# Kernel tuning notes

Measured on AMD Instinct MI355X. Metric: run time of the kernel, lower is better.

The kernel has to match this reference:

```python
import jax, jax.numpy as jnp
import numpy as np

B, D = 4096, 1024
NA, NNEG = 2048, 4094
L2_WEIGHT = 0.005


def setup_inputs() -> dict:
    key = jax.random.key(0)
    k1, k2, k3, k4 = jax.random.split(key, 4)
    batch = jax.random.normal(k1, (B, D), dtype=jnp.float32)
    anchors = jax.random.randint(k2, (NA,), 0, B)
    positives = jax.random.randint(k3, (NA,), 0, B)
    negatives = jax.random.randint(k4, (NA, NNEG), 0, B)
    return {"batch": batch, "anchors": anchors, "positives": positives, "negatives": negatives}


def reference(batch, anchors, positives, negatives):
    # a . (n - p) = a.n - a.p  -> one GEMM against the whole batch, then gathers.
    a_embs = batch[anchors]                       # [Na, D]
    scores = a_embs @ batch.T                     # [Na, B]
    pos = jnp.take_along_axis(scores, positives[:, None], axis=1)   # [Na, 1]
    neg = jnp.take_along_axis(scores, negatives, axis=1)            # [Na, Nneg]
    inner = neg - pos                             # [Na, Nneg]
    npair = jnp.mean(jnp.log(jnp.sum(jnp.exp(inner), axis=1) + 1.0))
    # per-anchor l2 term: l2_weight * mean(||batch||) added len(anchors) times / len(anchors)
    l2 = L2_WEIGHT * jnp.mean(jnp.linalg.norm(batch, axis=1))
    return npair + l2
```

## Files before the change

kernel.cpp:

```cpp
#include <hip/hip_runtime.h>
#include <hip/hip_bf16.h>
#include <math.h>

constexpr int kB    = 4096;
constexpr int kD    = 1024;
constexpr int kNA   = 2048;
constexpr int kNNEG = 4094;
constexpr float kL2W = 0.005f;


typedef __attribute__((ext_vector_type(8))) int   int8v;
typedef __attribute__((ext_vector_type(4))) int   int4v;
typedef __attribute__((ext_vector_type(4))) float f32x4;

__device__ inline void async_load16(const void* g, void* l) {
    __builtin_amdgcn_global_load_lds(
        (const __attribute__((address_space(1))) unsigned*)g,
        (__attribute__((address_space(3))) unsigned*)l, 16, 0, 0);
}
__device__ inline float bf16_to_f(unsigned short u) {
    union { unsigned int i; float f; } c; c.i = ((unsigned int)u) << 16; return c.f;
}

__global__ __launch_bounds__(256) void conv_norms_kernel(
    const float* __restrict__ batch,
    unsigned char* __restrict__ f8,
    float* __restrict__ norms)
{
    const int row = blockIdx.x, t = threadIdx.x;
    const float4 v = ((const float4*)(batch + (size_t)row * kD))[t];
    unsigned int p = __builtin_amdgcn_cvt_pk_fp8_f32(v.x, v.y, 0, false);
    p = __builtin_amdgcn_cvt_pk_fp8_f32(v.z, v.w, p, true);
    ((unsigned int*)(f8 + (size_t)row * kD))[t] = p;

    float acc = v.x * v.x + v.y * v.y + v.z * v.z + v.w * v.w;
    __shared__ float s[4];
    const int lane = t & 63, wid = t >> 6;
#pragma unroll
    for (int o2 = 32; o2; o2 >>= 1) acc += __shfl_down(acc, o2);
    if (lane == 0) s[wid] = acc;
    __syncthreads();
    if (t == 0) norms[row] = sqrtf(s[0] + s[1] + s[2] + s[3]);
}

__global__ __launch_bounds__(256) void gemm_mfma_kernel(
    const unsigned char* __restrict__ f8,
    const int*           __restrict__ anchors,
    unsigned short*      __restrict__ scores)
{
    __shared__ __align__(16) char As[128 * 128];
    __shared__ __align__(16) char Bs[128 * 128];
    __shared__ int aid[128];

    const int t  = threadIdx.x;
    const int w  = t >> 6;
    const int l  = t & 63;
    const int m0 = blockIdx.y * 128;
    const int n0 = blockIdx.x * 128;

    if (t < 128) aid[t] = anchors[m0 + t];
    __syncthreads();

    const unsigned char* gA[4];
    const unsigned char* gB[4];
    int slot[4];
#pragma unroll
    for (int i = 0; i < 4; ++i) {
        const int idx = i * 256 + t;
        const int row = idx >> 3;
        const int pc  = idx & 7;
        const int g   = pc ^ (row & 7);
        gA[i]   = f8 + (size_t)aid[row] * kD + g * 16;
        gB[i]   = f8 + (size_t)(n0 + row) * kD + g * 16;
        slot[i] = idx * 16;
    }

    const int wm = (w >> 1) * 64, wn = (w & 1) * 64;
    const int mr = l & 15, q = l >> 4;

    f32x4 acc[4][4] = {};

    for (int kt = 0; kt < kD; kt += 128) {
#pragma unroll
        for (int i = 0; i < 4; ++i) async_load16(gA[i] + kt, As + slot[i]);
#pragma unroll
        for (int i = 0; i < 4; ++i) async_load16(gB[i] + kt, Bs + slot[i]);
        __syncthreads();

        int8v a[4], b[4];
#pragma unroll
        for (int i = 0; i < 4; ++i) {
            int r  = wm + i * 16 + mr;
            int c0 = (2 * q) ^ (r & 7), c1 = (2 * q + 1) ^ (r & 7);
            int4v lo = *(const int4v*)(As + r * 128 + c0 * 16);
            int4v hi = *(const int4v*)(As + r * 128 + c1 * 16);
            a[i] = (int8v){lo.x, lo.y, lo.z, lo.w, hi.x, hi.y, hi.z, hi.w};
            r  = wn + i * 16 + mr;
            c0 = (2 * q) ^ (r & 7); c1 = (2 * q + 1) ^ (r & 7);
            lo = *(const int4v*)(Bs + r * 128 + c0 * 16);
            hi = *(const int4v*)(Bs + r * 128 + c1 * 16);
            b[i] = (int8v){lo.x, lo.y, lo.z, lo.w, hi.x, hi.y, hi.z, hi.w};
        }
#pragma unroll
        for (int i = 0; i < 4; ++i)
#pragma unroll
            for (int j = 0; j < 4; ++j)
                acc[i][j] = __builtin_amdgcn_mfma_scale_f32_16x16x128_f8f6f4(
                    a[i], b[j], acc[i][j],
                    0 , 0 ,
                    0, 0x7F ,
                    0, 0x7F );
        __syncthreads();
    }

#pragma unroll
    for (int i = 0; i < 4; ++i)
#pragma unroll
        for (int j = 0; j < 4; ++j)
#pragma unroll
            for (int r = 0; r < 4; ++r) {
                const int row = m0 + wm + i * 16 + q * 4 + r;
                const int col = n0 + wn + j * 16 + mr;
                __hip_bfloat16 h = __float2bfloat16(acc[i][j][r]);
                scores[(size_t)row * kB + col] = *(unsigned short*)&h;
            }
}

__global__ __launch_bounds__(256) void lse_kernel(
    const unsigned short* __restrict__ scores,
    const int*   __restrict__ positives,
    const int*   __restrict__ negatives,
    float*       __restrict__ lse)
{
    __shared__ unsigned short srow[kB];
    const int i = blockIdx.x;
    const int t = threadIdx.x;

    const uint4* grow = (const uint4*)(scores + (size_t)i * kB);
    ((uint4*)srow)[t]       = grow[t];
    ((uint4*)srow)[t + 256] = grow[t + 256];
    __syncthreads();

    const float pos = bf16_to_f(srow[positives[i]]);
    const int* negrow = negatives + (size_t)i * kNNEG;

    float v[16];
    float m = -INFINITY;
#pragma unroll
    for (int r = 0; r < 16; ++r) {
        const int j = t + 256 * r;
        v[r] = (j < kNNEG) ? (bf16_to_f(srow[negrow[j]]) - pos) : -INFINITY;
        m = fmaxf(m, v[r]);
    }

    __shared__ float sm[4], ss[4];
    const int lane = t & 63, wid = t >> 6;
#pragma unroll
    for (int o = 32; o; o >>= 1) m = fmaxf(m, __shfl_down(m, o));
    if (lane == 0) sm[wid] = m;
    __syncthreads();
    m = fmaxf(fmaxf(sm[0], sm[1]), fmaxf(sm[2], sm[3]));
    const float mp = fmaxf(m, 0.f);

    float acc = 0.f;
#pragma unroll
    for (int r = 0; r < 16; ++r) acc += expf(v[r] - mp);

#pragma unroll
    for (int o = 32; o; o >>= 1) acc += __shfl_down(acc, o);
    if (lane == 0) ss[wid] = acc;
    __syncthreads();
    if (t == 0)
        lse[i] = mp + logf(ss[0] + ss[1] + ss[2] + ss[3] + expf(-mp));
}

__global__ __launch_bounds__(256) void final_kernel(
    const float* __restrict__ lse,
    const float* __restrict__ norms,
    float*       __restrict__ out)
{
    float a = 0.f, b = 0.f;
    for (int i = threadIdx.x; i < kNA; i += 256) a += lse[i];
    for (int i = threadIdx.x; i < kB;  i += 256) b += norms[i];
    __shared__ float sa[4], sb[4];
    const int lane = threadIdx.x & 63, wid = threadIdx.x >> 6;
#pragma unroll
    for (int o = 32; o; o >>= 1) { a += __shfl_down(a, o); b += __shfl_down(b, o); }
    if (lane == 0) { sa[wid] = a; sb[wid] = b; }
    __syncthreads();
    if (threadIdx.x == 0) {
        const float npair = (sa[0] + sa[1] + sa[2] + sa[3]) / (float)kNA;
        const float l2    = kL2W * ((sb[0] + sb[1] + sb[2] + sb[3]) / (float)kB);
        out[0] = npair + l2;
    }
}

extern "C" void kernel_launch(void* const* d_in, const int* in_sizes, int n_in,
                              void* d_out, int out_size, void* d_ws, size_t ws_size,
                              hipStream_t stream)
{
    (void)in_sizes; (void)n_in; (void)out_size; (void)ws_size;

    const float* batch     = (const float*)d_in[0];
    const int*   anchors   = (const int*)d_in[1];
    const int*   positives = (const int*)d_in[2];
    const int*   negatives = (const int*)d_in[3];
    float*       out       = (float*)d_out;

    char* ws = (char*)d_ws;
    unsigned short* scores = (unsigned short*)ws;
    unsigned char*  f8     = (unsigned char*)(ws + (size_t)kNA * kB * 2);
    float*          lse    = (float*)(ws + (size_t)kNA * kB * 2 + (size_t)kB * kD);
    float*          norms  = lse + kNA;

    conv_norms_kernel<<<kB, 256, 0, stream>>>(batch, f8, norms);
    gemm_mfma_kernel<<<dim3(kB / 128, kNA / 128), 256, 0, stream>>>(f8, anchors, scores);
    lse_kernel<<<kNA, 256, 0, stream>>>(scores, positives, negatives, lse);
    final_kernel<<<1, 256, 0, stream>>>(lse, norms, out);
}
```

Baseline: 116.6 us.

## Fuse negative-weighted logsumexp into GEMM epilogue via per-anchor count histogram

Replaces the bf16 score matrix write and the gather-based LSE kernel with a per-anchor histogram of negative indices (uint8 counts), built in the same launch as the fp8 conversion. The GEMM epilogue then computes a count-weighted online max/sum-exp per row tile and emits partial (max, sum) pairs plus the positive score. A small merge kernel combines the partials and uses an atomic counter to do the final reduction. This removes the 16 MB score round-trip and the random gathers, at the cost of a heavier GEMM epilogue, shared-memory atomics and the assumption that each count fits in 8 bits.

```diff
diff --git a/kernel.cpp b/kernel.cpp
--- a/kernel.cpp
+++ b/kernel.cpp
@@ -18,35 +18,63 @@
         (const __attribute__((address_space(1))) unsigned*)g,
         (__attribute__((address_space(3))) unsigned*)l, 16, 0, 0);
 }
-__device__ inline float bf16_to_f(unsigned short u) {
-    union { unsigned int i; float f; } c; c.i = ((unsigned int)u) << 16; return c.f;
-}
-
-__global__ __launch_bounds__(256) void conv_norms_kernel(
+
+__global__ __launch_bounds__(256) void convhist_kernel(
     const float* __restrict__ batch,
+    const int*   __restrict__ negatives,
     unsigned char* __restrict__ f8,
-    float* __restrict__ norms)
-{
-    const int row = blockIdx.x, t = threadIdx.x;
-    const float4 v = ((const float4*)(batch + (size_t)row * kD))[t];
-    unsigned int p = __builtin_amdgcn_cvt_pk_fp8_f32(v.x, v.y, 0, false);
-    p = __builtin_amdgcn_cvt_pk_fp8_f32(v.z, v.w, p, true);
-    ((unsigned int*)(f8 + (size_t)row * kD))[t] = p;
-
-    float acc = v.x * v.x + v.y * v.y + v.z * v.z + v.w * v.w;
-    __shared__ float s[4];
-    const int lane = t & 63, wid = t >> 6;
-#pragma unroll
-    for (int o2 = 32; o2; o2 >>= 1) acc += __shfl_down(acc, o2);
-    if (lane == 0) s[wid] = acc;
-    __syncthreads();
-    if (t == 0) norms[row] = sqrtf(s[0] + s[1] + s[2] + s[3]);
+    unsigned char* __restrict__ cnt,
+    float* __restrict__ norms,
+    unsigned int* __restrict__ ctr)
+{
+    const int t = threadIdx.x;
+    if (blockIdx.x < kB) {
+        const int row = blockIdx.x;
+        const float4 v = ((const float4*)(batch + (size_t)row * kD))[t];
+        unsigned int p = __builtin_amdgcn_cvt_pk_fp8_f32(v.x, v.y, 0, false);
+        p = __builtin_amdgcn_cvt_pk_fp8_f32(v.z, v.w, p, true);
+        ((unsigned int*)(f8 + (size_t)row * kD))[t] = p;
+
+        float acc = v.x * v.x + v.y * v.y + v.z * v.z + v.w * v.w;
+        __shared__ float s[4];
+        const int lane = t & 63, wid = t >> 6;
+#pragma unroll
+        for (int o2 = 32; o2; o2 >>= 1) acc += __shfl_down(acc, o2);
+        if (lane == 0) s[wid] = acc;
+        __syncthreads();
+        if (t == 0) norms[row] = sqrtf(s[0] + s[1] + s[2] + s[3]);
+        if (blockIdx.x == 0 && t == 0) *ctr = 0;
+    } else {
+        const int i = blockIdx.x - kB;
+        __shared__ unsigned int h[kB];
+#pragma unroll
+        for (int r = 0; r < 16; ++r) h[t + 256 * r] = 0;
+        __syncthreads();
+        const int* negrow = negatives + (size_t)i * kNNEG;
+#pragma unroll
+        for (int r = 0; r < 16; ++r) {
+            const int j = t + 256 * r;
+            if (j < kNNEG) atomicAdd(&h[negrow[j]], 1u);
+        }
+        __syncthreads();
+        unsigned int w[4];
+#pragma unroll
+        for (int c = 0; c < 4; ++c) {
+            const int base = t * 16 + c * 4;
+            w[c] = (h[base] & 0xFFu) | ((h[base + 1] & 0xFFu) << 8) |
+                   ((h[base + 2] & 0xFFu) << 16) | ((h[base + 3] & 0xFFu) << 24);
+        }
+        ((uint4*)(cnt + (size_t)i * kB))[t] = make_uint4(w[0], w[1], w[2], w[3]);
+    }
 }
 
 __global__ __launch_bounds__(256) void gemm_mfma_kernel(
     const unsigned char* __restrict__ f8,
     const int*           __restrict__ anchors,
-    unsigned short*      __restrict__ scores)
+    const int*           __restrict__ positives,
+    const unsigned char* __restrict__ cnt,
+    float2*              __restrict__ part,
+    float*               __restrict__ posout)
 {
     __shared__ __align__(16) char As[128 * 128];
     __shared__ __align__(16) char Bs[128 * 128];
@@ -106,92 +134,111 @@
 #pragma unroll
             for (int j = 0; j < 4; ++j)
                 acc[i][j] = __builtin_amdgcn_mfma_scale_f32_16x16x128_f8f6f4(
-                    a[i], b[j], acc[i][j],
-                    0 , 0 ,
-                    0, 0x7F ,
-                    0, 0x7F );
-        __syncthreads();
-    }
-
-#pragma unroll
-    for (int i = 0; i < 4; ++i)
-#pragma unroll
-        for (int j = 0; j < 4; ++j)
-#pragma unroll
-            for (int r = 0; r < 4; ++r) {
-                const int row = m0 + wm + i * 16 + q * 4 + r;
-                const int col = n0 + wn + j * 16 + mr;
-                __hip_bfloat16 h = __float2bfloat16(acc[i][j][r]);
-                scores[(size_t)row * kB + col] = *(unsigned short*)&h;
+                    a[i], b[j], acc[i][j], 0, 0, 0, 0x7F, 0, 0x7F);
+        __syncthreads();
+    }
+
+    unsigned char* cntT = (unsigned char*)As;
+#pragma unroll
+    for (int i = 0; i < 4; ++i) {
+        const int idx = i * 256 + t;
+        const int row = idx >> 3;
+        const int c16 = idx & 7;
+        ((uint4*)cntT)[idx] =
+            *(const uint4*)(cnt + (size_t)(m0 + row) * kB + n0 + c16 * 16);
+    }
+    if (t < 128) aid[t] = positives[m0 + t];
+    __syncthreads();
+
+    float2* pm = (float2*)Bs;
+    const int half = wn >> 6;
+
+#pragma unroll
+    for (int i = 0; i < 4; ++i) {
+#pragma unroll
+        for (int r = 0; r < 4; ++r) {
+            const int rowL = wm + i * 16 + q * 4 + r;
+            float m4 = -1e30f;
+#pragma unroll
+            for (int j = 0; j < 4; ++j) {
+                const int colL = wn + j * 16 + mr;
+                const float s = acc[i][j][r];
+                if (cntT[rowL * 128 + colL] > 0) m4 = fmaxf(m4, s);
+                if (n0 + colL == aid[rowL]) posout[m0 + rowL] = s;
             }
-}
-
-__global__ __launch_bounds__(256) void lse_kernel(
-    const unsigned short* __restrict__ scores,
-    const int*   __restrict__ positives,
-    const int*   __restrict__ negatives,
-    float*       __restrict__ lse)
-{
-    __shared__ unsigned short srow[kB];
-    const int i = blockIdx.x;
+            float e4 = 0.f;
+#pragma unroll
+            for (int j = 0; j < 4; ++j) {
+                const int colL = wn + j * 16 + mr;
+                const float wgt = (float)cntT[rowL * 128 + colL];
+                const float e = (wgt > 0.f) ? __expf(acc[i][j][r] - m4) : 0.f;
+                e4 += wgt * e;
+            }
+            float M = m4, S = e4;
+#pragma unroll
+            for (int d = 1; d < 16; d <<= 1) {
+                const float Mo = __shfl_xor(M, d);
+                const float So = __shfl_xor(S, d);
+                const float Mn = fmaxf(M, Mo);
+                S = S * __expf(M - Mn) + So * __expf(Mo - Mn);
+                M = Mn;
+            }
+            if (mr == 0) pm[rowL * 2 + half] = make_float2(M, S);
+        }
+    }
+    __syncthreads();
+    if (t < 128) {
+        const float2 a0 = pm[t * 2], b0 = pm[t * 2 + 1];
+        const float M = fmaxf(a0.x, b0.x);
+        const float S = a0.y * __expf(a0.x - M) + b0.y * __expf(b0.x - M);
+        part[(size_t)(m0 + t) * 32 + blockIdx.x] = make_float2(M, S);
+    }
+}
+
+__global__ __launch_bounds__(256) void merge_kernel(
+    const float2* __restrict__ part,
+    const float*  __restrict__ posv,
+    const float*  __restrict__ norms,
+    float*        __restrict__ blocksums,
+    unsigned int* __restrict__ ctr,
+    float*        __restrict__ out)
+{
+    const int b = blockIdx.x;
     const int t = threadIdx.x;
 
-    const uint4* grow = (const uint4*)(scores + (size_t)i * kB);
-    ((uint4*)srow)[t]       = grow[t];
-    ((uint4*)srow)[t + 256] = grow[t + 256];
-    __syncthreads();
-
-    const float pos = bf16_to_f(srow[positives[i]]);
-    const int* negrow = negatives + (size_t)i * kNNEG;
-
-    float v[16];
-    float m = -INFINITY;
-#pragma unroll
-    for (int r = 0; r < 16; ++r) {
-        const int j = t + 256 * r;
-        v[r] = (j < kNNEG) ? (bf16_to_f(srow[negrow[j]]) - pos) : -INFINITY;
-        m = fmaxf(m, v[r]);
-    }
-
-    __shared__ float sm[4], ss[4];
+    float v = 0.f;
+    if (t < 128) {
+        const int row = b * 128 + t;
+        const float2* p = part + (size_t)row * 32;
+        float M = -1e30f;
+#pragma unroll
+        for (int c = 0; c < 32; ++c) M = fmaxf(M, p[c].x);
+        float S = 0.f;
+#pragma unroll
+        for (int c = 0; c < 32; ++c) S += p[c].y * __expf(p[c].x - M);
+        const float x = (M + logf(S)) - posv[row];
+        const float lse = (x > 0.f) ? (x + log1pf(__expf(-x))) : log1pf(__expf(x));
+        v = lse / (float)kNA;
+    }
+    v += kL2W * norms[b * 256 + t] / (float)kB;
+
+    __shared__ float s[4];
     const int lane = t & 63, wid = t >> 6;
 #pragma unroll
-    for (int o = 32; o; o >>= 1) m = fmaxf(m, __shfl_down(m, o));
-    if (lane == 0) sm[wid] = m;
-    __syncthreads();
-    m = fmaxf(fmaxf(sm[0], sm[1]), fmaxf(sm[2], sm[3]));
-    const float mp = fmaxf(m, 0.f);
-
-    float acc = 0.f;
-#pragma unroll
-    for (int r = 0; r < 16; ++r) acc += expf(v[r] - mp);
-
-#pragma unroll
-    for (int o = 32; o; o >>= 1) acc += __shfl_down(acc, o);
-    if (lane == 0) ss[wid] = acc;
-    __syncthreads();
-    if (t == 0)
-        lse[i] = mp + logf(ss[0] + ss[1] + ss[2] + ss[3] + expf(-mp));
-}
-
-__global__ __launch_bounds__(256) void final_kernel(
-    const float* __restrict__ lse,
-    const float* __restrict__ norms,
-    float*       __restrict__ out)
-{
-    float a = 0.f, b = 0.f;
-    for (int i = threadIdx.x; i < kNA; i += 256) a += lse[i];
-    for (int i = threadIdx.x; i < kB;  i += 256) b += norms[i];
-    __shared__ float sa[4], sb[4];
-    const int lane = threadIdx.x & 63, wid = threadIdx.x >> 6;
-#pragma unroll
-    for (int o = 32; o; o >>= 1) { a += __shfl_down(a, o); b += __shfl_down(b, o); }
-    if (lane == 0) { sa[wid] = a; sb[wid] = b; }
-    __syncthreads();
-    if (threadIdx.x == 0) {
-        const float npair = (sa[0] + sa[1] + sa[2] + sa[3]) / (float)kNA;
-        const float l2    = kL2W * ((sb[0] + sb[1] + sb[2] + sb[3]) / (float)kB);
-        out[0] = npair + l2;
+    for (int o = 32; o; o >>= 1) v += __shfl_down(v, o);
+    if (lane == 0) s[wid] = v;
+    __syncthreads();
+    if (t == 0) {
+        blocksums[b] = s[0] + s[1] + s[2] + s[3];
+        __threadfence();
+        const unsigned int old = atomicAdd(ctr, 1u);
+        if (old == 15u) {
+            __threadfence();
+            float tot = 0.f;
+#pragma unroll
+            for (int k = 0; k < 16; ++k) tot += blocksums[k];
+            out[0] = tot;
+        }
     }
 }
 
@@ -208,13 +255,16 @@
     float*       out       = (float*)d_out;
 
     char* ws = (char*)d_ws;
-    unsigned short* scores = (unsigned short*)ws;
-    unsigned char*  f8     = (unsigned char*)(ws + (size_t)kNA * kB * 2);
-    float*          lse    = (float*)(ws + (size_t)kNA * kB * 2 + (size_t)kB * kD);
-    float*          norms  = lse + kNA;
-
-    conv_norms_kernel<<<kB, 256, 0, stream>>>(batch, f8, norms);
-    gemm_mfma_kernel<<<dim3(kB / 128, kNA / 128), 256, 0, stream>>>(f8, anchors, scores);
-    lse_kernel<<<kNA, 256, 0, stream>>>(scores, positives, negatives, lse);
-    final_kernel<<<1, 256, 0, stream>>>(lse, norms, out);
-}
+    unsigned char* cnt    = (unsigned char*)ws;
+    unsigned char* f8     = (unsigned char*)(ws + (size_t)kNA * kB);
+    float2*        part   = (float2*)(ws + (size_t)kNA * kB + (size_t)kB * kD);
+    float*         posv   = (float*)((char*)part + (size_t)kNA * 32 * sizeof(float2));
+    float*         norms  = posv + kNA;
+    float*         bsums  = norms + kB;
+    unsigned int*  ctr    = (unsigned int*)(bsums + 16);
+
+    convhist_kernel<<<kB + kNA, 256, 0, stream>>>(batch, negatives, f8, cnt, norms, ctr);
+    gemm_mfma_kernel<<<dim3(kB / 128, kNA / 128), 256, 0, stream>>>(
+        f8, anchors, positives, cnt, part, posv);
+    merge_kernel<<<16, 256, 0, stream>>>(part, posv, norms, bsums, ctr, out);
+}
```

Result: slower. 135.9 us (+16.6%).

## Fold final reduction into atomics, async-load score rows, use fast exp/log

Applied to the files above, without the earlier changes.

Removes the final single-block reduction kernel. Per-row norm and per-anchor LSE contributions are now accumulated directly into the output with atomicAdd after a memset. The LSE kernel's score-row staging now uses global_load_lds async copies, and expf/logf become __expf/__logf. This trades one kernel launch for about 6K contended float atomics on a single address, adds a memset node, and makes the final sum order nondeterministic.

```diff
diff --git a/kernel.cpp b/kernel.cpp
--- a/kernel.cpp
+++ b/kernel.cpp
@@ -25,7 +25,7 @@
 __global__ __launch_bounds__(256) void conv_norms_kernel(
     const float* __restrict__ batch,
     unsigned char* __restrict__ f8,
-    float* __restrict__ norms)
+    float* __restrict__ out)
 {
     const int row = blockIdx.x, t = threadIdx.x;
     const float4 v = ((const float4*)(batch + (size_t)row * kD))[t];
@@ -40,7 +40,8 @@
     for (int o2 = 32; o2; o2 >>= 1) acc += __shfl_down(acc, o2);
     if (lane == 0) s[wid] = acc;
     __syncthreads();
-    if (t == 0) norms[row] = sqrtf(s[0] + s[1] + s[2] + s[3]);
+    if (t == 0)
+        atomicAdd(out, kL2W * sqrtf(s[0] + s[1] + s[2] + s[3]) / (float)kB);
 }
 
 __global__ __launch_bounds__(256) void gemm_mfma_kernel(
@@ -106,10 +107,7 @@
 #pragma unroll
             for (int j = 0; j < 4; ++j)
                 acc[i][j] = __builtin_amdgcn_mfma_scale_f32_16x16x128_f8f6f4(
-                    a[i], b[j], acc[i][j],
-                    0 , 0 ,
-                    0, 0x7F ,
-                    0, 0x7F );
+                    a[i], b[j], acc[i][j], 0, 0, 0, 0x7F, 0, 0x7F);
         __syncthreads();
     }
 
@@ -130,15 +128,15 @@
     const unsigned short* __restrict__ scores,
     const int*   __restrict__ positives,
     const int*   __restrict__ negatives,
-    float*       __restrict__ lse)
+    float*       __restrict__ out)
 {
-    __shared__ unsigned short srow[kB];
+    __shared__ __align__(16) unsigned short srow[kB];
     const int i = blockIdx.x;
     const int t = threadIdx.x;
 
-    const uint4* grow = (const uint4*)(scores + (size_t)i * kB);
-    ((uint4*)srow)[t]       = grow[t];
-    ((uint4*)srow)[t + 256] = grow[t + 256];
+    const unsigned char* grow = (const unsigned char*)(scores + (size_t)i * kB);
+    async_load16(grow + t * 16,          (char*)srow + t * 16);
+    async_load16(grow + (t + 256) * 16,  (char*)srow + (t + 256) * 16);
     __syncthreads();
 
     const float pos = bf16_to_f(srow[positives[i]]);
@@ -164,34 +162,15 @@
 
     float acc = 0.f;
 #pragma unroll
-    for (int r = 0; r < 16; ++r) acc += expf(v[r] - mp);
+    for (int r = 0; r < 16; ++r) acc += __expf(v[r] - mp);
 
 #pragma unroll
     for (int o = 32; o; o >>= 1) acc += __shfl_down(acc, o);
     if (lane == 0) ss[wid] = acc;
     __syncthreads();
-    if (t == 0)
-        lse[i] = mp + logf(ss[0] + ss[1] + ss[2] + ss[3] + expf(-mp));
-}
-
-__global__ __launch_bounds__(256) void final_kernel(
-    const float* __restrict__ lse,
-    const float* __restrict__ norms,
-    float*       __restrict__ out)
-{
-    float a = 0.f, b = 0.f;
-    for (int i = threadIdx.x; i < kNA; i += 256) a += lse[i];
-    for (int i = threadIdx.x; i < kB;  i += 256) b += norms[i];
-    __shared__ float sa[4], sb[4];
-    const int lane = threadIdx.x & 63, wid = threadIdx.x >> 6;
-#pragma unroll
-    for (int o = 32; o; o >>= 1) { a += __shfl_down(a, o); b += __shfl_down(b, o); }
-    if (lane == 0) { sa[wid] = a; sb[wid] = b; }
-    __syncthreads();
-    if (threadIdx.x == 0) {
-        const float npair = (sa[0] + sa[1] + sa[2] + sa[3]) / (float)kNA;
-        const float l2    = kL2W * ((sb[0] + sb[1] + sb[2] + sb[3]) / (float)kB);
-        out[0] = npair + l2;
+    if (t == 0) {
+        const float lse = mp + __logf(ss[0] + ss[1] + ss[2] + ss[3] + __expf(-mp));
+        atomicAdd(out, lse / (float)kNA);
     }
 }
 
@@ -210,11 +189,9 @@
     char* ws = (char*)d_ws;
     unsigned short* scores = (unsigned short*)ws;
     unsigned char*  f8     = (unsigned char*)(ws + (size_t)kNA * kB * 2);
-    float*          lse    = (float*)(ws + (size_t)kNA * kB * 2 + (size_t)kB * kD);
-    float*          norms  = lse + kNA;
 
-    conv_norms_kernel<<<kB, 256, 0, stream>>>(batch, f8, norms);
+    hipMemsetAsync(out, 0, sizeof(float), stream);
+    conv_norms_kernel<<<kB, 256, 0, stream>>>(batch, f8, out);
     gemm_mfma_kernel<<<dim3(kB / 128, kNA / 128), 256, 0, stream>>>(f8, anchors, scores);
-    lse_kernel<<<kNA, 256, 0, stream>>>(scores, positives, negatives, lse);
-    final_kernel<<<1, 256, 0, stream>>>(lse, norms, out);
+    lse_kernel<<<kNA, 256, 0, stream>>>(scores, positives, negatives, out);
 }
```

New measurement: 182.6 us. 56.6% more time.
